# Kernel tuning notes

Measured on AMD Instinct MI355X. Metric: run time of the kernel, lower is better.

## Reference

```python
import jax, jax.numpy as jnp
import numpy as np

B, T, I, H, K = 32, 1024, 512, 512, 2


def _causal_conv1d(x_bit, w_hik, b_h):
    # x_bit: [B, I, T]; left-pad K-1 zeros (ConstantPad1d((K-1, 0)))
    xp = jnp.pad(x_bit, ((0, 0), (0, 0), (K - 1, 0)))
    y = jax.lax.conv_general_dilated(
        xp, w_hik, window_strides=(1,), padding='VALID',
        dimension_numbers=('NCH', 'OIH', 'NCH'))  # [B, H, T]
    return y + b_h[None, :, None]


def setup_inputs() -> dict:
    key = jax.random.key(0)
    k1, k2, k3 = jax.random.split(key, 3)
    bound = 1.0 / np.sqrt(I * K)  # torch Conv1d default init scale
    return {
        'inputs': jax.random.normal(k1, (B, T, I), dtype=jnp.float32),
        'init_state': jnp.zeros((B, H), dtype=jnp.float32),
        'Wz': jax.random.uniform(k2, (H, I, K), jnp.float32, -bound, bound),
        'bz': jnp.zeros((H,), dtype=jnp.float32),
        'Wf': jax.random.uniform(k3, (H, I, K), jnp.float32, -bound, bound),
        'bf': jnp.zeros((H,), dtype=jnp.float32),
    }


def reference(inputs, init_state, Wz, bz, Wf, bf):
    # init_state is accepted but unused in the original forward (mode='f').
    x = inputs.transpose(0, 2, 1)                      # [B, I, T]
    raw_f = _causal_conv1d(x, Wf, bf).transpose(0, 2, 1)  # [B, T, H]
    raw_z = _causal_conv1d(x, Wz, bz).transpose(0, 2, 1)  # [B, T, H]

    log_f = jax.nn.log_sigmoid(raw_f)
    log_one_minus_f = jax.nn.log_sigmoid(-raw_f)
    log_z = jax.nn.log_sigmoid(raw_z)

    # recurrent_gates[t] = sum_{s>t} log_f[s]  (suffix sum of log_f over time, excluding t=0 shift)
    rg = log_f[:, 1:, :]                               # [B, T-1, H]
    cs = jnp.cumsum(rg, axis=1)
    rg = rg - cs + cs[:, -1:, :]
    rg = jnp.concatenate([rg, jnp.zeros((inputs.shape[0], 1, rg.shape[2]), dtype=rg.dtype)], axis=1)  # [B, T, H]

    log_hidden = jax.lax.cumlogsumexp(log_z + log_one_minus_f + rg, axis=1)
    hidden = jnp.exp(log_hidden - rg)
    return hidden
```

## Files before the change

kernel.cpp:

```cpp
#include <hip/hip_runtime.h>
#include <hip/hip_bf16.h>
#include <cstddef>
#include <cstdint>

#define B_  32
#define T_  1024
#define I_  512
#define H_  512
#define M_  (B_ * T_)
#define TP_ 1025

typedef __bf16 bf16x8  __attribute__((ext_vector_type(8)));
typedef float  floatx4 __attribute__((ext_vector_type(4)));
typedef unsigned short ushort8v __attribute__((ext_vector_type(8)));
typedef unsigned long long u64;

__device__ __forceinline__ unsigned short f2bf(float f) {
    uint32_t u = __float_as_uint(f);
    return (unsigned short)((u + 0x7FFFu + ((u >> 16) & 1u)) >> 16);
}
__device__ __forceinline__ float sigm(float x) {
    return __builtin_amdgcn_rcpf(1.f + __expf(-x));
}

#define GLL(src, dst) __builtin_amdgcn_global_load_lds( \
    (const __attribute__((address_space(1))) void*)(src), \
    (__attribute__((address_space(3))) void*)(dst), 16, 0, 0)

#define NB_BUILD 8200
#define NB_PACK  512
#define NB_ZERO  256

__global__ __launch_bounds__(256) void prep(const float* __restrict__ x,
                                            const float* __restrict__ Wf,
                                            const float* __restrict__ Wz,
                                            unsigned short* __restrict__ Ab2,
                                            unsigned short* __restrict__ Wq,
                                            uint4* __restrict__ HpubZ,
                                            uint32_t* __restrict__ tickets) {
    if (blockIdx.x < NB_BUILD) {
        int g = blockIdx.x * 256 + threadIdx.x;
        int idx8 = g << 3;
        int row = idx8 >> 9;
        int col = idx8 & 511;
        int b    = (int)((unsigned)row / TP_);
        int trow = row - b * TP_;
        ushort8v o = {0, 0, 0, 0, 0, 0, 0, 0};
        if (trow > 0) {
            const float* src = &x[((size_t)b * T_ + (trow - 1)) * I_ + col];
            float4 v0 = *(const float4*)src;
            float4 v1 = *(const float4*)(src + 4);
            o[0] = f2bf(v0.x); o[1] = f2bf(v0.y); o[2] = f2bf(v0.z); o[3] = f2bf(v0.w);
            o[4] = f2bf(v1.x); o[5] = f2bf(v1.y); o[6] = f2bf(v1.z); o[7] = f2bf(v1.w);
        }
        *(ushort8v*)&Ab2[(size_t)idx8] = o;
    } else if (blockIdx.x < NB_BUILD + NB_PACK) {
        int cid = (blockIdx.x - NB_BUILD) * 256 + threadIdx.x;
        int lane = cid & 63;
        int c    = (cid >> 6) & 3;
        int wn   = (cid >> 8) & 1;
        int ksub = (cid >> 9) & 31;
        int ni   = (cid >> 14) & 3;
        int gate = (cid >> 16) & 1;
        int n_col = ni * 128 + wn * 64 + c * 16 + (lane & 15);
        const float* G = gate ? Wz : Wf;
        ushort8v o;
        #pragma unroll
        for (int j = 0; j < 8; ++j) {
            int k   = ksub * 32 + (lane >> 4) * 8 + j;
            int tap = k >> 9;
            int i   = k & 511;
            o[j] = f2bf(G[n_col * (I_ * 2) + i * 2 + tap]);
        }
        *(ushort8v*)&Wq[(size_t)cid * 8] = o;
    } else {
        int g = (blockIdx.x - NB_BUILD - NB_PACK) * 256 + threadIdx.x;
        HpubZ[g] = make_uint4(0, 0, 0, 0);
        if (g < 128) tickets[g] = 0;
    }
}

__global__ __launch_bounds__(256, 2) void mfma_gemm_scan(
        const unsigned short* __restrict__ Ab2,
        const unsigned short* __restrict__ Wq,
        const float* __restrict__ biasF,
        const float* __restrict__ biasZ,
        float* __restrict__ out,
        u64* __restrict__ Hpub,
        uint32_t* __restrict__ tickets) {
    __shared__ unsigned short smem[24576];
    __shared__ uint32_t pos_s;

    const int tid = threadIdx.x;
    const int bid = blockIdx.x;
    const int x   = bid & 7;
    const int ni  = (bid >> 3) & 3;
    const int q   = bid >> 5;
    const int b   = ((q & 3) << 3) | x;
    const int chain = ni * 32 + b;
    if (tid == 0) pos_s = atomicAdd(&tickets[chain], 1u);
    __syncthreads();
    const int pos = (int)pos_s;
    const int h0  = ni * 128;
    const int browBase = b * TP_ + pos * 128;

    const int lane = tid & 63;
    const int wave = tid >> 6;
    const int wm   = wave >> 1, wn = wave & 1;
    const int lm   = lane & 15, quad = lane >> 4;

    const int c0 = wave * 128 + lane;
    const int c1 = c0 + 64;
    const int r0 = c0 >> 2, q0 = (c0 & 3) ^ ((r0 >> 2) & 3);
    const int r1 = c1 >> 2, q1 = (c1 & 3) ^ ((r1 >> 2) & 3);

    const unsigned short* pA0 = Ab2 + (size_t)(browBase + r0) * 512 + q0 * 8;
    const unsigned short* pA1 = Ab2 + (size_t)(browBase + r1) * 512 + q1 * 8;

    const unsigned short* pBF = Wq + ni * 131072 + wn * 2048 + lane * 8;

    int offA[4];
    #pragma unroll
    for (int r = 0; r < 4; ++r) {
        int ml = wm * 64 + r * 16 + lm;
        offA[r] = (4 * ml + (quad ^ ((ml >> 2) & 3))) * 8;
    }

    floatx4 accF[4][4] = {};
    floatx4 accZ[4][4] = {};
    bf16x8 bfA[4], bzA[4], bfB[4], bzB[4];

#define ISSUE_A(ksub, sA) do {                                          \
        const int aoff_ = (((ksub) >> 4) * 512) + (((ksub) & 15) * 32); \
        GLL(pA0 + aoff_, (sA) + wave * 1024);                           \
        GLL(pA1 + aoff_, (sA) + wave * 1024 + 512);                     \
    } while (0)

#define LOADB(ksub, BF, BZ) do {                                        \
        const unsigned short* pf_ = pBF + (ksub) * 4096;                \
        _Pragma("unroll")                                               \
        for (int c = 0; c < 4; ++c) {                                   \
            BF[c] = *(const bf16x8*)(pf_ + c * 512);                    \
            BZ[c] = *(const bf16x8*)(pf_ + 524288 + c * 512);           \
        }                                                               \
    } while (0)

#define MFMA32(AF, BF, BZ) do {                                         \
        __builtin_amdgcn_s_setprio(1);                                  \
        _Pragma("unroll")                                               \
        for (int r = 0; r < 4; ++r) {                                   \
            _Pragma("unroll")                                           \
            for (int c = 0; c < 4; ++c) {                               \
                accF[r][c] = __builtin_amdgcn_mfma_f32_16x16x32_bf16(   \
                                AF[r], BF[c], accF[r][c], 0, 0, 0);     \
                accZ[r][c] = __builtin_amdgcn_mfma_f32_16x16x32_bf16(   \
                                AF[r], BZ[c], accZ[r][c], 0, 0, 0);     \
            }                                                           \
        }                                                               \
        __builtin_amdgcn_s_setprio(0);                                  \
    } while (0)

#define RDA(slot, AF) do {                                              \
        _Pragma("unroll")                                               \
        for (int r = 0; r < 4; ++r)                                     \
            AF[r] = *(const bf16x8*)((slot) + offA[r]);                 \
    } while (0)

#define ROT() do { unsigned short* t_ = s0; s0 = s1; s1 = s2; s2 = t_; } while (0)

    unsigned short* s0 = smem;
    unsigned short* s1 = smem + 4096;
    unsigned short* s2 = smem + 8192;

    ISSUE_A(0, s0);
    ISSUE_A(1, s1);
    LOADB(0, bfA, bzA);

    {
        asm volatile("s_waitcnt vmcnt(0)");
        __builtin_amdgcn_s_barrier();
        asm volatile("" ::: "memory");
        bf16x8 af_[4];
        RDA(s0, af_);
        LOADB(1, bfB, bzB);
        ISSUE_A(2, s2);
        __builtin_amdgcn_sched_barrier(0);
        MFMA32(af_, bfA, bzA);
        ROT();
    }
    for (int p = 0; p < 14; ++p) {
        const int k1 = 2 * p + 1;
        {
            asm volatile("s_waitcnt vmcnt(2)");
            __builtin_amdgcn_s_barrier();
            asm volatile("" ::: "memory");
            bf16x8 af_[4];
            RDA(s0, af_);
            LOADB(k1 + 1, bfA, bzA);
            ISSUE_A(k1 + 2, s2);
            __builtin_amdgcn_sched_barrier(0);
            MFMA32(af_, bfB, bzB);
            ROT();
        }
        {
            asm volatile("s_waitcnt vmcnt(2)");
            __builtin_amdgcn_s_barrier();
            asm volatile("" ::: "memory");
            bf16x8 af_[4];
            RDA(s0, af_);
            LOADB(k1 + 2, bfB, bzB);
            ISSUE_A(k1 + 3, s2);
            __builtin_amdgcn_sched_barrier(0);
            MFMA32(af_, bfA, bzA);
            ROT();
        }
    }
    {
        asm volatile("s_waitcnt vmcnt(2)");
        __builtin_amdgcn_s_barrier();
        asm volatile("" ::: "memory");
        bf16x8 af_[4];
        RDA(s0, af_);
        LOADB(30, bfA, bzA);
        ISSUE_A(31, s2);
        __builtin_amdgcn_sched_barrier(0);
        MFMA32(af_, bfB, bzB);
        ROT();
    }
    {
        asm volatile("s_waitcnt vmcnt(2)");
        __builtin_amdgcn_s_barrier();
        asm volatile("" ::: "memory");
        bf16x8 af_[4];
        RDA(s0, af_);
        LOADB(31, bfB, bzB);
        __builtin_amdgcn_sched_barrier(0);
        MFMA32(af_, bfA, bzA);
        ROT();
    }
    {
        asm volatile("s_waitcnt vmcnt(0)");
        __builtin_amdgcn_s_barrier();
        asm volatile("" ::: "memory");
        bf16x8 af_[4];
        RDA(s0, af_);
        __builtin_amdgcn_sched_barrier(0);
        MFMA32(af_, bfB, bzB);
    }
#undef ISSUE_A
#undef LOADB
#undef MFMA32
#undef RDA
#undef ROT
    __syncthreads();

    float bfv[4], bzv[4];
    #pragma unroll
    for (int c = 0; c < 4; ++c) {
        int hc = h0 + wn * 64 + c * 16 + lm;
        bfv[c] = biasF[hc];
        bzv[c] = biasZ[hc];
    }

    float2* seg  = (float2*)smem;
    float*  hinL = (float*)&smem[16384];

    #pragma unroll
    for (int r = 0; r < 4; ++r) {
        const int sid = wm * 16 + r * 4 + quad;
        #pragma unroll
        for (int c = 0; c < 4; ++c) {
            float A = 1.f, C = 0.f;
            #pragma unroll
            for (int v = 0; v < 4; ++v) {
                float f = sigm(accF[r][c][v] + bfv[c]);
                float z = sigm(accZ[r][c][v] + bzv[c]);
                accF[r][c][v] = f;
                accZ[r][c][v] = z;
                A *= f;
                C = fmaf(f, C - z, z);
            }
            seg[sid * 128 + wn * 64 + c * 16 + lm] = make_float2(A, C);
        }
    }
    __syncthreads();

    if (tid < 128) {
        float At = 1.f, Ct = 0.f;
        #pragma unroll 8
        for (int s = 0; s < 32; ++s) {
            float2 sc = seg[s * 128 + tid];
            Ct = fmaf(sc.x, Ct, sc.y);
            At *= sc.x;
        }
        float Hin = 0.f;
        if (pos > 0) {
            u64* p = &Hpub[((size_t)(pos - 1) * 128 + chain) * 128 + tid];
            u64 v;
            while (((v = atomicAdd(p, 0ull)) >> 32) == 0ull)
                __builtin_amdgcn_s_sleep(2);
            Hin = __uint_as_float((uint32_t)v);
        }
        if (pos < 7) {
            float Hout = fmaf(At, Hin, Ct);
            u64 pv = 0x100000000ull | (u64)__float_as_uint(Hout);
            atomicExch(&Hpub[((size_t)pos * 128 + chain) * 128 + tid], pv);
        }
        float run = Hin;
        #pragma unroll 8
        for (int s = 0; s < 32; ++s) {
            hinL[s * 128 + tid] = run;
            float2 sc = seg[s * 128 + tid];
            run = fmaf(sc.x, run, sc.y);
        }
    }
    __syncthreads();

    const int rowBase = b * T_ + pos * 128;
    #pragma unroll
    for (int r = 0; r < 4; ++r) {
        const int sid = wm * 16 + r * 4 + quad;
        #pragma unroll
        for (int c = 0; c < 4; ++c) {
            const int hc = h0 + wn * 64 + c * 16 + lm;
            float hs = hinL[sid * 128 + (hc - h0)];
            #pragma unroll
            for (int v = 0; v < 4; ++v) {
                float f = accF[r][c][v];
                float z = accZ[r][c][v];
                hs = fmaf(f, hs - z, z);
                const size_t row = (size_t)(rowBase + wm * 64 + r * 16 + quad * 4 + v);
                out[row * H_ + hc] = hs;
            }
        }
    }
}

extern "C" void kernel_launch(void* const* d_in, const int* in_sizes, int n_in,
                              void* d_out, int out_size, void* d_ws, size_t ws_size,
                              hipStream_t stream) {
    const float* x  = (const float*)d_in[0];
    const float* Wz = (const float*)d_in[2];
    const float* bz = (const float*)d_in[3];
    const float* Wf = (const float*)d_in[4];
    const float* bf = (const float*)d_in[5];
    float* out = (float*)d_out;

    char* ws = (char*)d_ws;
    unsigned short* Ab2  = (unsigned short*)(ws);
    unsigned short* Wq   = (unsigned short*)(ws + (size_t)34 * 1024 * 1024);
    u64*            Hpub = (u64*)(ws + (size_t)36 * 1024 * 1024);
    uint32_t*       tkt  = (uint32_t*)(ws + (size_t)37 * 1024 * 1024);

    prep<<<NB_BUILD + NB_PACK + NB_ZERO, 256, 0, stream>>>(
        x, Wf, Wz, Ab2, Wq, (uint4*)Hpub, tkt);

    mfma_gemm_scan<<<1024, 256, 0, stream>>>(Ab2, Wq, bf, bz, out, Hpub, tkt);
}
```

Baseline: 193.4 us.

## Halve per-block H tile to 64 columns and raise occupancy to three blocks per CU

Each block now computes a 128x64 output tile per gate instead of 128x128, halving accumulators and B-fragment registers. The grid doubles to 2048 blocks, the chain count to 256, and launch bounds ask for 3 blocks per SIMD group, with shared memory shrunk to match. The aim is more resident waves to hide memory and scan-handoff latency. The cost is that every A tile is loaded twice as often, with less MFMA work per A load, and there are twice as many cross-block scan chains. The prologue wait is also relaxed to vmcnt(2).

```diff
diff --git a/kernel.cpp b/kernel.cpp
--- a/kernel.cpp
+++ b/kernel.cpp
@@ -76,11 +76,11 @@
     } else {
         int g = (blockIdx.x - NB_BUILD - NB_PACK) * 256 + threadIdx.x;
         HpubZ[g] = make_uint4(0, 0, 0, 0);
-        if (g < 128) tickets[g] = 0;
-    }
-}
-
-__global__ __launch_bounds__(256, 2) void mfma_gemm_scan(
+        if (g < 256) tickets[g] = 0;
+    }
+}
+
+__global__ __launch_bounds__(256, 3) void mfma_gemm_scan(
         const unsigned short* __restrict__ Ab2,
         const unsigned short* __restrict__ Wq,
         const float* __restrict__ biasF,
@@ -88,25 +88,26 @@
         float* __restrict__ out,
         u64* __restrict__ Hpub,
         uint32_t* __restrict__ tickets) {
-    __shared__ unsigned short smem[24576];
+    __shared__ unsigned short smem[12288];
     __shared__ uint32_t pos_s;
 
     const int tid = threadIdx.x;
     const int bid = blockIdx.x;
     const int x   = bid & 7;
-    const int ni  = (bid >> 3) & 3;
-    const int q   = bid >> 5;
+    const int nh  = (bid >> 3) & 7;
+    const int q   = bid >> 6;
     const int b   = ((q & 3) << 3) | x;
-    const int chain = ni * 32 + b;
+    const int chain = nh * 32 + b;
     if (tid == 0) pos_s = atomicAdd(&tickets[chain], 1u);
     __syncthreads();
     const int pos = (int)pos_s;
-    const int h0  = ni * 128;
+    const int h0  = nh * 64;
     const int browBase = b * TP_ + pos * 128;
 
     const int lane = tid & 63;
     const int wave = tid >> 6;
-    const int wm   = wave >> 1, wn = wave & 1;
+    const int wm   = wave >> 1;
+    const int wh   = wave & 1;
     const int lm   = lane & 15, quad = lane >> 4;
 
     const int c0 = wave * 128 + lane;
@@ -117,7 +118,8 @@
     const unsigned short* pA0 = Ab2 + (size_t)(browBase + r0) * 512 + q0 * 8;
     const unsigned short* pA1 = Ab2 + (size_t)(browBase + r1) * 512 + q1 * 8;
 
-    const unsigned short* pBF = Wq + ni * 131072 + wn * 2048 + lane * 8;
+    const unsigned short* pBF = Wq + (size_t)(nh >> 1) * 131072
+                                   + (nh & 1) * 2048 + wh * 1024 + lane * 8;
 
     int offA[4];
     #pragma unroll
@@ -126,9 +128,9 @@
         offA[r] = (4 * ml + (quad ^ ((ml >> 2) & 3))) * 8;
     }
 
-    floatx4 accF[4][4] = {};
-    floatx4 accZ[4][4] = {};
-    bf16x8 bfA[4], bzA[4], bfB[4], bzB[4];
+    floatx4 accF[4][2] = {};
+    floatx4 accZ[4][2] = {};
+    bf16x8 bfA[2], bzA[2], bfB[2], bzB[2];
 
 #define ISSUE_A(ksub, sA) do {                                          \
         const int aoff_ = (((ksub) >> 4) * 512) + (((ksub) & 15) * 32); \
@@ -138,19 +140,18 @@
 
 #define LOADB(ksub, BF, BZ) do {                                        \
         const unsigned short* pf_ = pBF + (ksub) * 4096;                \
-        _Pragma("unroll")                                               \
-        for (int c = 0; c < 4; ++c) {                                   \
-            BF[c] = *(const bf16x8*)(pf_ + c * 512);                    \
-            BZ[c] = *(const bf16x8*)(pf_ + 524288 + c * 512);           \
-        }                                                               \
+        BF[0] = *(const bf16x8*)(pf_);                                  \
+        BF[1] = *(const bf16x8*)(pf_ + 512);                            \
+        BZ[0] = *(const bf16x8*)(pf_ + 524288);                         \
+        BZ[1] = *(const bf16x8*)(pf_ + 524288 + 512);                   \
     } while (0)
 
-#define MFMA32(AF, BF, BZ) do {                                         \
+#define MFMA16(AF, BF, BZ) do {                                         \
         __builtin_amdgcn_s_setprio(1);                                  \
         _Pragma("unroll")                                               \
         for (int r = 0; r < 4; ++r) {                                   \
             _Pragma("unroll")                                           \
-            for (int c = 0; c < 4; ++c) {                               \
+            for (int c = 0; c < 2; ++c) {                               \
                 accF[r][c] = __builtin_amdgcn_mfma_f32_16x16x32_bf16(   \
                                 AF[r], BF[c], accF[r][c], 0, 0, 0);     \
                 accZ[r][c] = __builtin_amdgcn_mfma_f32_16x16x32_bf16(   \
@@ -173,11 +174,11 @@
     unsigned short* s2 = smem + 8192;
 
     ISSUE_A(0, s0);
+    LOADB(0, bfA, bzA);
     ISSUE_A(1, s1);
-    LOADB(0, bfA, bzA);
 
     {
-        asm volatile("s_waitcnt vmcnt(0)");
+        asm volatile("s_waitcnt vmcnt(2)");
         __builtin_amdgcn_s_barrier();
         asm volatile("" ::: "memory");
         bf16x8 af_[4];
@@ -185,7 +186,7 @@
         LOADB(1, bfB, bzB);
         ISSUE_A(2, s2);
         __builtin_amdgcn_sched_barrier(0);
-        MFMA32(af_, bfA, bzA);
+        MFMA16(af_, bfA, bzA);
         ROT();
     }
     for (int p = 0; p < 14; ++p) {
@@ -199,7 +200,7 @@
             LOADB(k1 + 1, bfA, bzA);
             ISSUE_A(k1 + 2, s2);
             __builtin_amdgcn_sched_barrier(0);
-            MFMA32(af_, bfB, bzB);
+            MFMA16(af_, bfB, bzB);
             ROT();
         }
         {
@@ -211,7 +212,7 @@
             LOADB(k1 + 2, bfB, bzB);
             ISSUE_A(k1 + 3, s2);
             __builtin_amdgcn_sched_barrier(0);
-            MFMA32(af_, bfA, bzA);
+            MFMA16(af_, bfA, bzA);
             ROT();
         }
     }
@@ -224,7 +225,7 @@
         LOADB(30, bfA, bzA);
         ISSUE_A(31, s2);
         __builtin_amdgcn_sched_barrier(0);
-        MFMA32(af_, bfB, bzB);
+        MFMA16(af_, bfB, bzB);
         ROT();
     }
     {
@@ -235,7 +236,7 @@
         RDA(s0, af_);
         LOADB(31, bfB, bzB);
         __builtin_amdgcn_sched_barrier(0);
-        MFMA32(af_, bfA, bzA);
+        MFMA16(af_, bfA, bzA);
         ROT();
     }
     {
@@ -245,31 +246,31 @@
         bf16x8 af_[4];
         RDA(s0, af_);
         __builtin_amdgcn_sched_barrier(0);
-        MFMA32(af_, bfB, bzB);
+        MFMA16(af_, bfB, bzB);
     }
 #undef ISSUE_A
 #undef LOADB
-#undef MFMA32
+#undef MFMA16
 #undef RDA
 #undef ROT
     __syncthreads();
 
-    float bfv[4], bzv[4];
+    float bfv[2], bzv[2];
     #pragma unroll
-    for (int c = 0; c < 4; ++c) {
-        int hc = h0 + wn * 64 + c * 16 + lm;
+    for (int c = 0; c < 2; ++c) {
+        int hc = h0 + wh * 32 + c * 16 + lm;
         bfv[c] = biasF[hc];
         bzv[c] = biasZ[hc];
     }
 
     float2* seg  = (float2*)smem;
-    float*  hinL = (float*)&smem[16384];
+    float*  hinL = (float*)&smem[8192];
 
     #pragma unroll
     for (int r = 0; r < 4; ++r) {
         const int sid = wm * 16 + r * 4 + quad;
         #pragma unroll
-        for (int c = 0; c < 4; ++c) {
+        for (int c = 0; c < 2; ++c) {
             float A = 1.f, C = 0.f;
             #pragma unroll
             for (int v = 0; v < 4; ++v) {
@@ -280,22 +281,23 @@
                 A *= f;
                 C = fmaf(f, C - z, z);
             }
-            seg[sid * 128 + wn * 64 + c * 16 + lm] = make_float2(A, C);
+            seg[sid * 64 + wh * 32 + c * 16 + lm] = make_float2(A, C);
         }
     }
     __syncthreads();
 
-    if (tid < 128) {
+    if (tid < 64) {
+        const int h = tid;
         float At = 1.f, Ct = 0.f;
         #pragma unroll 8
         for (int s = 0; s < 32; ++s) {
-            float2 sc = seg[s * 128 + tid];
+            float2 sc = seg[s * 64 + h];
             Ct = fmaf(sc.x, Ct, sc.y);
             At *= sc.x;
         }
         float Hin = 0.f;
         if (pos > 0) {
-            u64* p = &Hpub[((size_t)(pos - 1) * 128 + chain) * 128 + tid];
+            u64* p = &Hpub[((size_t)(pos - 1) * 256 + chain) * 64 + h];
             u64 v;
             while (((v = atomicAdd(p, 0ull)) >> 32) == 0ull)
                 __builtin_amdgcn_s_sleep(2);
@@ -304,13 +306,13 @@
         if (pos < 7) {
             float Hout = fmaf(At, Hin, Ct);
             u64 pv = 0x100000000ull | (u64)__float_as_uint(Hout);
-            atomicExch(&Hpub[((size_t)pos * 128 + chain) * 128 + tid], pv);
+            atomicExch(&Hpub[((size_t)pos * 256 + chain) * 64 + h], pv);
         }
         float run = Hin;
         #pragma unroll 8
         for (int s = 0; s < 32; ++s) {
-            hinL[s * 128 + tid] = run;
-            float2 sc = seg[s * 128 + tid];
+            hinL[s * 64 + h] = run;
+            float2 sc = seg[s * 64 + h];
             run = fmaf(sc.x, run, sc.y);
         }
     }
@@ -321,16 +323,16 @@
     for (int r = 0; r < 4; ++r) {
         const int sid = wm * 16 + r * 4 + quad;
         #pragma unroll
-        for (int c = 0; c < 4; ++c) {
-            const int hc = h0 + wn * 64 + c * 16 + lm;
-            float hs = hinL[sid * 128 + (hc - h0)];
+        for (int c = 0; c < 2; ++c) {
+            const int hcl = wh * 32 + c * 16 + lm;
+            float hs = hinL[sid * 64 + hcl];
             #pragma unroll
             for (int v = 0; v < 4; ++v) {
                 float f = accF[r][c][v];
                 float z = accZ[r][c][v];
                 hs = fmaf(f, hs - z, z);
                 const size_t row = (size_t)(rowBase + wm * 64 + r * 16 + quad * 4 + v);
-                out[row * H_ + hc] = hs;
+                out[row * H_ + h0 + hcl] = hs;
             }
         }
     }
@@ -355,5 +357,5 @@
     prep<<<NB_BUILD + NB_PACK + NB_ZERO, 256, 0, stream>>>(
         x, Wf, Wz, Ab2, Wq, (uint4*)Hpub, tkt);
 
-    mfma_gemm_scan<<<1024, 256, 0, stream>>>(Ab2, Wq, bf, bz, out, Hpub, tkt);
-}
+    mfma_gemm_scan<<<2048, 256, 0, stream>>>(Ab2, Wq, bf, bz, out, Hpub, tkt);
+}
```

Measured after the change: 203.2 us. 5.1% more time.
